# Performance work log

Hardware: AMD Instinct MI355X
Metric: run time of the kernel (lower is better)

Reference implementation:

```python
import jax, jax.numpy as jnp
import numpy as np

N_NODES = 50000
N_EDGES = 800000
DIMS = [128, 512, 256, 128]
EPS = 1e-5


def setup_inputs() -> dict:
    key = jax.random.key(0)
    ks = jax.random.split(key, 2 + 5 * 3)
    inp = {
        "x": jax.random.normal(ks[0], (N_NODES, DIMS[0]), dtype=jnp.float32),
        "edge_index": jax.random.randint(ks[1], (2, N_EDGES), 0, N_NODES, dtype=jnp.int64),
    }
    ki = 2
    for i in range(3):
        din, dout = DIMS[i], DIMS[i + 1]
        s = 1.0 / np.sqrt(din)
        inp[f"Wl{i}"] = jax.random.uniform(ks[ki + 0], (din, dout), jnp.float32, -s, s)
        inp[f"bl{i}"] = jax.random.uniform(ks[ki + 1], (dout,), jnp.float32, -s, s)
        inp[f"Wr{i}"] = jax.random.uniform(ks[ki + 2], (din, dout), jnp.float32, -s, s)
        inp[f"g{i}"] = jnp.ones((dout,), jnp.float32)
        inp[f"b{i}"] = jnp.zeros((dout,), jnp.float32)
        ki += 5
    return inp


def _sage_mean(x, src, dst, Wl, bl, Wr):
    n = x.shape[0]
    agg = jax.ops.segment_sum(x[src], dst, num_segments=n)  # [N, din]
    deg = jax.ops.segment_sum(jnp.ones((src.shape[0],), x.dtype), dst, num_segments=n)
    mean = agg / jnp.maximum(deg, 1.0)[:, None]
    return mean @ Wl + bl + x @ Wr


def _bn(h, gamma, beta):
    m = h.mean(axis=0)
    v = h.var(axis=0)
    return gamma * (h - m) * jax.lax.rsqrt(v + EPS) + beta


def reference(x, edge_index, Wl0, bl0, Wr0, g0, b0, Wl1, bl1, Wr1, g1, b1, Wl2, bl2, Wr2, g2, b2):
    src, dst = edge_index[0], edge_index[1]
    params = [(Wl0, bl0, Wr0, g0, b0), (Wl1, bl1, Wr1, g1, b1), (Wl2, bl2, Wr2, g2, b2)]
    h = x
    for Wl, bl, Wr, g, b in params:
        h = _sage_mean(h, src, dst, Wl, bl, Wr)
        h = _bn(h, g, b)
        h = jax.nn.relu(h)
        # dropout: identity in eval mode
    return h
```

## Files before the change

kernel.cpp:

```cpp
#include <hip/hip_runtime.h>
#include <cstdint>
#include <cstddef>


#define EPS_BN 1e-5f

typedef unsigned short ushort_t;
typedef __attribute__((ext_vector_type(8))) short short8;
typedef __attribute__((ext_vector_type(4))) float float4v;

__device__ __forceinline__ float bf2f(ushort_t u) {
    union { unsigned int i; float f; } v; v.i = ((unsigned int)u) << 16; return v.f;
}
__device__ __forceinline__ ushort_t f2bf(float f) {
    union { float f; unsigned int i; } v; v.f = f;
    unsigned int r = v.i + 0x7fffu + ((v.i >> 16) & 1u);
    return (ushort_t)(r >> 16);
}

__device__ __forceinline__ void async_copy16(void* lds, const void* g) {
    __builtin_amdgcn_global_load_lds(
        (const __attribute__((address_space(1))) unsigned int*)g,
        (__attribute__((address_space(3))) unsigned int*)lds, 16, 0, 0);
}

__global__ void detect_fmt_kernel(const int* __restrict__ edges, int* __restrict__ nz) {
    int t = threadIdx.x;
    int cnt = 0;
    #pragma unroll
    for (int j = 0; j < 4; ++j) {
        int idx = 2 * (t * 4 + j) + 1;
        if (edges[idx] != 0) cnt++;
    }
    if (cnt) atomicAdd(nz, cnt);
}

__device__ __forceinline__ void edge_sd(const int* __restrict__ p, int e, int ne,
                                        bool is64, int& s, int& d) {
    if (is64) { s = p[2 * e];  d = p[2 * ne + 2 * e]; }
    else      { s = p[e];      d = p[ne + e]; }
}

__global__ void count_deg_kernel(const int* __restrict__ edges, int ne,
                                 const int* __restrict__ nz, int* __restrict__ degi) {
    bool is64 = (*nz == 0);
    int e = blockIdx.x * 256 + threadIdx.x;
    if (e < ne) {
        int s, d; edge_sd(edges, e, ne, is64, s, d);
        atomicAdd(&degi[d], 1);
    }
}

__global__ void scan1_kernel(const int* __restrict__ degi, int n,
                             int* __restrict__ rowptr, int* __restrict__ bsums) {
    __shared__ int sh[1024];
    int t = threadIdx.x;
    int i = blockIdx.x * 1024 + t;
    int v = (i < n) ? degi[i] : 0;
    sh[t] = v;
    __syncthreads();
    for (int off = 1; off < 1024; off <<= 1) {
        int x = (t >= off) ? sh[t - off] : 0;
        __syncthreads();
        sh[t] += x;
        __syncthreads();
    }
    if (i < n) rowptr[i] = sh[t] - v;
    if (t == 1023) bsums[blockIdx.x] = sh[t];
}

__global__ void scan2_kernel(int* __restrict__ bsums, int nb,
                             int* __restrict__ rowptr, int n, int total) {
    if (threadIdx.x == 0 && blockIdx.x == 0) {
        int run = 0;
        for (int b = 0; b < nb; ++b) { int t = bsums[b]; bsums[b] = run; run += t; }
        rowptr[n] = total;
    }
}

__global__ void scan3_kernel(int* __restrict__ rowptr, int n,
                             const int* __restrict__ bsums, int* __restrict__ cursor) {
    int i = blockIdx.x * 1024 + threadIdx.x;
    if (i < n) {
        int v = rowptr[i] + bsums[blockIdx.x];
        rowptr[i] = v;
        cursor[i] = v;
    }
}

__global__ void scatter_kernel(const int* __restrict__ edges, int ne,
                               const int* __restrict__ nz,
                               int* __restrict__ cursor, int* __restrict__ csr_src) {
    bool is64 = (*nz == 0);
    int e = blockIdx.x * 256 + threadIdx.x;
    if (e < ne) {
        int s, d; edge_sd(edges, e, ne, is64, s, d);
        int pos = atomicAdd(&cursor[d], 1);
        csr_src[pos] = s;
    }
}

__global__ void f2b_kernel(const float* __restrict__ in, ushort_t* __restrict__ out, int n) {
    int i = blockIdx.x * 256 + threadIdx.x;
    if (i < n) out[i] = f2bf(in[i]);
}

__global__ void prep_wt_kernel(const float* __restrict__ Wl, const float* __restrict__ Wr,
                               ushort_t* __restrict__ WT, int K1, int Dout) {
    int idx = blockIdx.x * 256 + threadIdx.x;
    int K2 = 2 * K1;
    if (idx >= Dout * K2) return;
    int n = idx / K2, k = idx - n * K2;
    float v = (k < K1) ? Wl[(size_t)k * Dout + n] : Wr[(size_t)(k - K1) * Dout + n];
    WT[idx] = f2bf(v);
}

__global__ void prep_wtc_kernel(const float* __restrict__ Wl, const float* __restrict__ Wr,
                                ushort_t* __restrict__ WTc, int K, int D) {
    int idx = blockIdx.x * 256 + threadIdx.x;
    if (idx >= 2 * D * K) return;
    int nn = idx / K, k = idx - nn * K;
    float v = (nn < D) ? Wl[(size_t)k * D + nn] : Wr[(size_t)k * D + (nn - D)];
    WTc[idx] = f2bf(v);
}

template <int VEC> struct VecT;
template <> struct VecT<2> { using T = unsigned int; };
template <> struct VecT<4> { using T = uint2; };
template <> struct VecT<8> { using T = uint4; };

template <int VEC>
__device__ __forceinline__ void vunpack(typename VecT<VEC>::T v, unsigned int* w) {
    if constexpr (VEC == 2) { w[0] = v; }
    else if constexpr (VEC == 4) { w[0] = v.x; w[1] = v.y; }
    else { w[0] = v.x; w[1] = v.y; w[2] = v.z; w[3] = v.w; }
}

template <int VEC>
__device__ __forceinline__ void vaccum(typename VecT<VEC>::T v, float* acc) {
    unsigned int w[VEC / 2];
    vunpack<VEC>(v, w);
    #pragma unroll
    for (int i = 0; i < VEC / 2; ++i) {
        acc[2 * i + 0] += bf2f((ushort_t)(w[i] & 0xffffu));
        acc[2 * i + 1] += bf2f((ushort_t)(w[i] >> 16));
    }
}

template <int VEC>
__device__ __forceinline__ void gather_sum(
    const ushort_t* __restrict__ base, const int* __restrict__ csr_src,
    int e0, int e1, int rstride, float* acc) {
    using VT = typename VecT<VEC>::T;
    int e = e0;
    for (; e + 8 <= e1; e += 8) {
        VT v[8];
        #pragma unroll
        for (int u = 0; u < 8; ++u)
            v[u] = *(const VT*)(base + (size_t)csr_src[e + u] * rstride);
        #pragma unroll
        for (int u = 0; u < 8; ++u) vaccum<VEC>(v[u], acc);
    }
    if (e + 4 <= e1) {
        VT v[4];
        #pragma unroll
        for (int u = 0; u < 4; ++u)
            v[u] = *(const VT*)(base + (size_t)csr_src[e + u] * rstride);
        #pragma unroll
        for (int u = 0; u < 4; ++u) vaccum<VEC>(v[u], acc);
        e += 4;
    }
    if (e + 2 <= e1) {
        VT v0 = *(const VT*)(base + (size_t)csr_src[e] * rstride);
        VT v1 = *(const VT*)(base + (size_t)csr_src[e + 1] * rstride);
        vaccum<VEC>(v0, acc); vaccum<VEC>(v1, acc);
        e += 2;
    }
    if (e < e1)
        vaccum<VEC>(*(const VT*)(base + (size_t)csr_src[e] * rstride), acc);
}

template <int VEC>
__global__ __launch_bounds__(256) void aggregate_wave_kernel(
    const ushort_t* __restrict__ h, ushort_t* __restrict__ mean,
    const int* __restrict__ rowptr, const int* __restrict__ csr_src, int nnodes) {
    const int din = VEC * 64;
    int wid = blockIdx.x * 4 + (threadIdx.x >> 6);
    if (wid >= nnodes) return;
    int lane = threadIdx.x & 63;
    int e0 = rowptr[wid], e1 = rowptr[wid + 1];

    float acc[VEC];
    #pragma unroll
    for (int i = 0; i < VEC; ++i) acc[i] = 0.f;
    gather_sum<VEC>(h + (size_t)lane * VEC, csr_src, e0, e1, din, acc);

    int deg = e1 - e0;
    float scale = 1.0f / (float)(deg > 1 ? deg : 1);
    unsigned int o[VEC / 2];
    #pragma unroll
    for (int i = 0; i < VEC / 2; ++i)
        o[i] = (unsigned int)f2bf(acc[2 * i] * scale) |
               ((unsigned int)f2bf(acc[2 * i + 1] * scale) << 16);
    using VT = typename VecT<VEC>::T;
    VT ov;
    if constexpr (VEC == 2) { ov = o[0]; }
    else if constexpr (VEC == 4) { ov.x = o[0]; ov.y = o[1]; }
    else { ov.x = o[0]; ov.y = o[1]; ov.z = o[2]; ov.w = o[3]; }
    *(VT*)(mean + (size_t)wid * din + (size_t)lane * VEC) = ov;
}

template <int VEC>
__global__ __launch_bounds__(256) void aggregate_add_kernel(
    const ushort_t* __restrict__ PR, const float* __restrict__ bias,
    ushort_t* __restrict__ pre,
    const int* __restrict__ rowptr, const int* __restrict__ csr_src, int nnodes) {
    const int D = VEC * 64;
    const int stride = 2 * D;
    int wid = blockIdx.x * 4 + (threadIdx.x >> 6);
    if (wid >= nnodes) return;
    int lane = threadIdx.x & 63;
    int e0 = rowptr[wid], e1 = rowptr[wid + 1];

    float acc[VEC];
    #pragma unroll
    for (int i = 0; i < VEC; ++i) acc[i] = 0.f;
    gather_sum<VEC>(PR + (size_t)lane * VEC, csr_src, e0, e1, stride, acc);

    int deg = e1 - e0;
    float scale = 1.0f / (float)(deg > 1 ? deg : 1);

    using VT = typename VecT<VEC>::T;
    VT rv = *(const VT*)(PR + (size_t)wid * stride + D + (size_t)lane * VEC);
    unsigned int rw[VEC / 2];
    vunpack<VEC>(rv, rw);
    float o[VEC];
    #pragma unroll
    for (int i = 0; i < VEC / 2; ++i) {
        o[2 * i + 0] = bf2f((ushort_t)(rw[i] & 0xffffu));
        o[2 * i + 1] = bf2f((ushort_t)(rw[i] >> 16));
    }
    #pragma unroll
    for (int i = 0; i < VEC; ++i)
        o[i] += acc[i] * scale + bias[lane * VEC + i];

    unsigned int ow[VEC / 2];
    #pragma unroll
    for (int i = 0; i < VEC / 2; ++i)
        ow[i] = (unsigned int)f2bf(o[2 * i]) | ((unsigned int)f2bf(o[2 * i + 1]) << 16);
    VT ov;
    if constexpr (VEC == 2) { ov = ow[0]; }
    else if constexpr (VEC == 4) { ov.x = ow[0]; ov.y = ow[1]; }
    else { ov.x = ow[0]; ov.y = ow[1]; ov.z = ow[2]; ov.w = ow[3]; }
    *(VT*)(pre + (size_t)wid * D + (size_t)lane * VEC) = ov;
}

template <bool DUAL, bool BIAS>
__global__ __launch_bounds__(256) void gemm_glds_kernel(
    const ushort_t* __restrict__ A1, const ushort_t* __restrict__ A2,
    const ushort_t* __restrict__ BT, const float* __restrict__ bias,
    ushort_t* __restrict__ Cb, int N, int K1, int Ktot, int Wtot) {
    __shared__ ushort_t As[128 * 32];
    __shared__ ushort_t Bs[128 * 32];

    const int tid = threadIdx.x;
    const int wave = tid >> 6;
    const int lane = tid & 63;
    const int quad = lane >> 4;
    const int l15 = lane & 15;
    const int rowBase = blockIdx.y * 128;
    const int colBase = blockIdx.x * 128;
    const int wm = (wave >> 1) * 64;
    const int wn = (wave & 1) * 64;
    const int swz = (l15 >> 1) & 3;

    float4v acc[4][4];
    #pragma unroll
    for (int i = 0; i < 4; ++i)
        #pragma unroll
        for (int j = 0; j < 4; ++j)
            acc[i][j] = (float4v){0.f, 0.f, 0.f, 0.f};

    const int nkt = Ktot / 32;
    const int khalf = K1 / 32;

    for (int kt = 0; kt < nkt; ++kt) {
        const ushort_t* Asrc = A1;
        int kg = kt * 32;
        if (DUAL && kt >= khalf) { Asrc = A2; kg = (kt - khalf) * 32; }
        const int kb = kt * 32;

        #pragma unroll
        for (int u = 0; u < 2; ++u) {
            int c = u * 256 + tid;
            int r = c >> 2;
            int off = (((c & 3) ^ ((c >> 3) & 3)) * 8);
            int grow = rowBase + r;
            if (grow >= N) grow = N - 1;
            async_copy16(&As[c * 8], Asrc + (size_t)grow * K1 + kg + off);
            async_copy16(&Bs[c * 8], BT + (size_t)(colBase + r) * Ktot + kb + off);
        }
        __syncthreads();

        short8 af[4], bf4[4];
        #pragma unroll
        for (int i = 0; i < 4; ++i)
            af[i] = *(const short8*)&As[(wm + i * 16 + l15) * 32 + (quad ^ swz) * 8];
        #pragma unroll
        for (int j = 0; j < 4; ++j)
            bf4[j] = *(const short8*)&Bs[(wn + j * 16 + l15) * 32 + (quad ^ swz) * 8];

        #pragma unroll
        for (int i = 0; i < 4; ++i)
            #pragma unroll
            for (int j = 0; j < 4; ++j)
                acc[i][j] = __builtin_amdgcn_mfma_f32_16x16x32_bf16(bf4[j], af[i], acc[i][j], 0, 0, 0);
        __syncthreads();
    }

    ushort_t* lws = (wave < 2) ? &As[wave * 2048] : &Bs[(wave - 2) * 2048];
    #pragma unroll
    for (int p = 0; p < 2; ++p) {
        #pragma unroll
        for (int jj = 0; jj < 2; ++jj) {
            int j = 2 * p + jj;
            float4 bv = make_float4(0.f, 0.f, 0.f, 0.f);
            if (BIAS) bv = *(const float4*)(bias + colBase + wn + j * 16 + quad * 4);
            #pragma unroll
            for (int i = 0; i < 4; ++i) {
                uint2 pk;
                pk.x = (unsigned int)f2bf(acc[i][j][0] + bv.x) |
                       ((unsigned int)f2bf(acc[i][j][1] + bv.y) << 16);
                pk.y = (unsigned int)f2bf(acc[i][j][2] + bv.z) |
                       ((unsigned int)f2bf(acc[i][j][3] + bv.w) << 16);
                *(uint2*)&lws[(i * 16 + l15) * 32 + jj * 16 + quad * 4] = pk;
            }
        }
        __syncthreads();
        #pragma unroll
        for (int it = 0; it < 4; ++it) {
            int c = it * 64 + lane;
            int row = c >> 2, coff = (c & 3) * 8;
            int grow = rowBase + wm + row;
            if (grow < N) {
                uint4 v = *(const uint4*)&lws[row * 32 + coff];
                *(uint4*)(Cb + (size_t)grow * Wtot + colBase + wn + p * 32 + coff) = v;
            }
        }
        __syncthreads();
    }
}

__global__ void colstats_b_kernel(const ushort_t* __restrict__ h, int N, int D,
                                  float* __restrict__ sum, float* __restrict__ sumsq) {
    int c2 = blockIdx.x * 128 + (threadIdx.x & 63) * 2;
    int rl = threadIdx.x >> 6;
    float s0 = 0.f, s20 = 0.f, s1 = 0.f, s21 = 0.f;
    int stride = gridDim.y * 4;
    for (int r = blockIdx.y * 4 + rl; r < N; r += stride) {
        unsigned int w = *(const unsigned int*)(h + (size_t)r * D + c2);
        float v0 = bf2f((ushort_t)(w & 0xffffu));
        float v1 = bf2f((ushort_t)(w >> 16));
        s0 += v0; s20 += v0 * v0;
        s1 += v1; s21 += v1 * v1;
    }
    atomicAdd(&sum[c2 + 0], s0);
    atomicAdd(&sumsq[c2 + 0], s20);
    atomicAdd(&sum[c2 + 1], s1);
    atomicAdd(&sumsq[c2 + 1], s21);
}

__global__ void bn_relu_b2b_kernel(const ushort_t* __restrict__ h, ushort_t* __restrict__ hb,
                                   int N, int D,
                                   const float* __restrict__ sum, const float* __restrict__ sumsq,
                                   const float* __restrict__ g, const float* __restrict__ b) {
    size_t idx = (size_t)blockIdx.x * blockDim.x + threadIdx.x;
    size_t tot = (size_t)N * D / 2;
    if (idx >= tot) return;
    int cp = (int)(idx & (size_t)(D / 2 - 1));
    int c0 = cp * 2, c1 = c0 + 1;
    float m0 = sum[c0] / (float)N, m1 = sum[c1] / (float)N;
    float i0 = rsqrtf(sumsq[c0] / (float)N - m0 * m0 + EPS_BN);
    float i1 = rsqrtf(sumsq[c1] / (float)N - m1 * m1 + EPS_BN);
    unsigned int w = ((const unsigned int*)h)[idx];
    float v0 = g[c0] * (bf2f((ushort_t)(w & 0xffffu)) - m0) * i0 + b[c0];
    float v1 = g[c1] * (bf2f((ushort_t)(w >> 16)) - m1) * i1 + b[c1];
    v0 = v0 > 0.f ? v0 : 0.f;
    v1 = v1 > 0.f ? v1 : 0.f;
    ((unsigned int*)hb)[idx] = (unsigned int)f2bf(v0) | ((unsigned int)f2bf(v1) << 16);
}

__global__ void bn_relu_b2f_kernel(const ushort_t* __restrict__ h, float* __restrict__ hf,
                                   int N, int D,
                                   const float* __restrict__ sum, const float* __restrict__ sumsq,
                                   const float* __restrict__ g, const float* __restrict__ b) {
    size_t idx = (size_t)blockIdx.x * blockDim.x + threadIdx.x;
    size_t tot = (size_t)N * D / 2;
    if (idx >= tot) return;
    int cp = (int)(idx & (size_t)(D / 2 - 1));
    int c0 = cp * 2, c1 = c0 + 1;
    float m0 = sum[c0] / (float)N, m1 = sum[c1] / (float)N;
    float i0 = rsqrtf(sumsq[c0] / (float)N - m0 * m0 + EPS_BN);
    float i1 = rsqrtf(sumsq[c1] / (float)N - m1 * m1 + EPS_BN);
    unsigned int w = ((const unsigned int*)h)[idx];
    float v0 = g[c0] * (bf2f((ushort_t)(w & 0xffffu)) - m0) * i0 + b[c0];
    float v1 = g[c1] * (bf2f((ushort_t)(w >> 16)) - m1) * i1 + b[c1];
    float2 o;
    o.x = v0 > 0.f ? v0 : 0.f;
    o.y = v1 > 0.f ? v1 : 0.f;
    *(float2*)(hf + idx * 2) = o;
}

extern "C" void kernel_launch(void* const* d_in, const int* in_sizes, int n_in,
                              void* d_out, int out_size, void* d_ws, size_t ws_size,
                              hipStream_t stream) {
    const float* x     = (const float*)d_in[0];
    const int*   edges = (const int*)d_in[1];
    const float* Wl0 = (const float*)d_in[2];
    const float* bl0 = (const float*)d_in[3];
    const float* Wr0 = (const float*)d_in[4];
    const float* g0  = (const float*)d_in[5];
    const float* b0  = (const float*)d_in[6];
    const float* Wl1 = (const float*)d_in[7];
    const float* bl1 = (const float*)d_in[8];
    const float* Wr1 = (const float*)d_in[9];
    const float* g1  = (const float*)d_in[10];
    const float* b1  = (const float*)d_in[11];
    const float* Wl2 = (const float*)d_in[12];
    const float* bl2 = (const float*)d_in[13];
    const float* Wr2 = (const float*)d_in[14];
    const float* g2  = (const float*)d_in[15];
    const float* b2  = (const float*)d_in[16];

    const int D0 = 128, D1 = 512, D2 = 256, D3 = 128;
    const int n  = in_sizes[0] / D0;
    const int ne = in_sizes[1] / 2;

    char* base = (char*)d_ws;
    size_t off = 0;
    auto alloc = [&](size_t bytes) -> char* {
        char* p = base + off;
        off = (off + bytes + 255) & ~(size_t)255;
        return p;
    };
    int*      nzflag  = (int*)alloc(4);
    int*      degi    = (int*)alloc((size_t)n * 4);
    float*    stats   = (float*)alloc(6 * 512 * 4);
    size_t    zero_span = off;
    int*      rowptr  = (int*)alloc((size_t)(n + 1) * 4);
    int*      cursor  = (int*)alloc((size_t)n * 4);
    int*      csr_src = (int*)alloc((size_t)ne * 4);
    int*      bsums   = (int*)alloc(64 * 4);
    ushort_t* xb      = (ushort_t*)alloc((size_t)n * D0 * 2);
    ushort_t* mb      = (ushort_t*)alloc((size_t)n * 512 * 2);
    ushort_t* h1b     = (ushort_t*)alloc((size_t)n * D1 * 2);
    ushort_t* h2b     = (ushort_t*)alloc((size_t)n * D2 * 2);
    ushort_t* hpre    = (ushort_t*)alloc((size_t)n * 512 * 2);
    ushort_t* WT0     = (ushort_t*)alloc((size_t)D1 * 2 * D0 * 2);
    ushort_t* WT1c    = (ushort_t*)alloc((size_t)(2 * D2) * D1 * 2);
    ushort_t* WT2c    = (ushort_t*)alloc((size_t)(2 * D3) * D2 * 2);
    float*    out     = (float*)d_out;
    (void)ws_size; (void)n_in; (void)out_size;

    hipMemsetAsync(base, 0, zero_span, stream);

    detect_fmt_kernel<<<1, 256, 0, stream>>>(edges, nzflag);
    count_deg_kernel<<<(ne + 255) / 256, 256, 0, stream>>>(edges, ne, nzflag, degi);
    int nscan = (n + 1023) / 1024;
    scan1_kernel<<<nscan, 1024, 0, stream>>>(degi, n, rowptr, bsums);
    scan2_kernel<<<1, 64, 0, stream>>>(bsums, nscan, rowptr, n, ne);
    scan3_kernel<<<nscan, 1024, 0, stream>>>(rowptr, n, bsums, cursor);
    scatter_kernel<<<(ne + 255) / 256, 256, 0, stream>>>(edges, ne, nzflag, cursor, csr_src);

    f2b_kernel<<<((size_t)n * D0 + 255) / 256, 256, 0, stream>>>(x, xb, n * D0);
    prep_wt_kernel<<<(D1 * 2 * D0 + 255) / 256, 256, 0, stream>>>(Wl0, Wr0, WT0, D0, D1);
    prep_wtc_kernel<<<(2 * D2 * D1 + 255) / 256, 256, 0, stream>>>(Wl1, Wr1, WT1c, D1, D2);
    prep_wtc_kernel<<<(2 * D3 * D2 + 255) / 256, 256, 0, stream>>>(Wl2, Wr2, WT2c, D2, D3);

    const int aggGrid = (n + 3) / 4;
    const int rowBlocks = (n + 127) / 128;
    float* st0 = stats + 0 * 1024;
    float* st1 = stats + 1 * 1024;
    float* st2 = stats + 2 * 1024;

    aggregate_wave_kernel<2><<<aggGrid, 256, 0, stream>>>(xb, mb, rowptr, csr_src, n);
    gemm_glds_kernel<true, true><<<dim3(D1 / 128, rowBlocks), 256, 0, stream>>>(
        mb, xb, WT0, bl0, hpre, n, D0, 2 * D0, D1);
    colstats_b_kernel<<<dim3(D1 / 128, 128), 256, 0, stream>>>(hpre, n, D1, st0, st0 + 512);
    bn_relu_b2b_kernel<<<((size_t)n * D1 / 2 + 255) / 256, 256, 0, stream>>>(
        hpre, h1b, n, D1, st0, st0 + 512, g0, b0);

    gemm_glds_kernel<false, false><<<dim3(2 * D2 / 128, rowBlocks), 256, 0, stream>>>(
        h1b, nullptr, WT1c, nullptr, mb, n, D1, D1, 2 * D2);
    aggregate_add_kernel<4><<<aggGrid, 256, 0, stream>>>(
        mb, bl1, hpre, rowptr, csr_src, n);
    colstats_b_kernel<<<dim3(D2 / 128, 128), 256, 0, stream>>>(hpre, n, D2, st1, st1 + 512);
    bn_relu_b2b_kernel<<<((size_t)n * D2 / 2 + 255) / 256, 256, 0, stream>>>(
        hpre, h2b, n, D2, st1, st1 + 512, g1, b1);

    gemm_glds_kernel<false, false><<<dim3(2 * D3 / 128, rowBlocks), 256, 0, stream>>>(
        h2b, nullptr, WT2c, nullptr, mb, n, D2, D2, 2 * D3);
    aggregate_add_kernel<2><<<aggGrid, 256, 0, stream>>>(
        mb, bl2, hpre, rowptr, csr_src, n);
    colstats_b_kernel<<<dim3(D3 / 128, 128), 256, 0, stream>>>(hpre, n, D3, st2, st2 + 512);
    bn_relu_b2f_kernel<<<((size_t)n * D3 / 2 + 255) / 256, 256, 0, stream>>>(
        hpre, out, n, D3, st2, st2 + 512, g2, b2);
}
```

Baseline: 666.0 us.

## Build CSR via two-level bucket sort and widen GEMM K-tile to 64

Replaces the global-atomic degree count, three-kernel scan and per-edge atomic scatter with a bucketed counting sort. Edges are grouped by dst>>8 using LDS histograms, packed with the low dst bits, and each bucket is then sorted locally to produce rowptr and csr_src. This cuts global atomic contention and kernel launches. Separately, the GEMM K-tile grows from 32 to 64 with a wider XOR swizzle, halving the barrier count per K, at the cost of doubled LDS use and lower occupancy. The packing assumes source indices fit in 24 bits and at most 256 buckets, so n is limited to about 65536.

```diff
diff --git a/kernel.cpp b/kernel.cpp
--- a/kernel.cpp
+++ b/kernel.cpp
@@ -40,63 +40,116 @@
     if (is64) { s = p[2 * e];  d = p[2 * ne + 2 * e]; }
     else      { s = p[e];      d = p[ne + e]; }
 }
-
-__global__ void count_deg_kernel(const int* __restrict__ edges, int ne,
-                                 const int* __restrict__ nz, int* __restrict__ degi) {
+__device__ __forceinline__ int edge_d(const int* __restrict__ p, int e, int ne, bool is64) {
+    return is64 ? p[2 * ne + 2 * e] : p[ne + e];
+}
+
+#define EPB 2048
+
+__global__ __launch_bounds__(256) void bhist_kernel(
+    const int* __restrict__ edges, int ne, const int* __restrict__ nz,
+    int* __restrict__ gcnt) {
+    __shared__ int h[256];
+    int t = threadIdx.x;
+    h[t] = 0;
+    __syncthreads();
     bool is64 = (*nz == 0);
-    int e = blockIdx.x * 256 + threadIdx.x;
-    if (e < ne) {
-        int s, d; edge_sd(edges, e, ne, is64, s, d);
-        atomicAdd(&degi[d], 1);
-    }
-}
-
-__global__ void scan1_kernel(const int* __restrict__ degi, int n,
-                             int* __restrict__ rowptr, int* __restrict__ bsums) {
-    __shared__ int sh[1024];
+    int base_e = blockIdx.x * EPB;
+    #pragma unroll
+    for (int u = 0; u < EPB / 256; ++u) {
+        int i = base_e + u * 256 + t;
+        if (i < ne) atomicAdd(&h[edge_d(edges, i, ne, is64) >> 8], 1);
+    }
+    __syncthreads();
+    if (h[t]) atomicAdd(&gcnt[t], h[t]);
+}
+
+__global__ __launch_bounds__(256) void bscan_kernel(
+    const int* __restrict__ gcnt, int nb, int ne,
+    int* __restrict__ bbase, int* __restrict__ bcur) {
+    __shared__ int sh[256];
     int t = threadIdx.x;
-    int i = blockIdx.x * 1024 + t;
-    int v = (i < n) ? degi[i] : 0;
+    int v = (t < nb) ? gcnt[t] : 0;
     sh[t] = v;
     __syncthreads();
-    for (int off = 1; off < 1024; off <<= 1) {
-        int x = (t >= off) ? sh[t - off] : 0;
+    for (int o = 1; o < 256; o <<= 1) {
+        int x = (t >= o) ? sh[t - o] : 0;
         __syncthreads();
         sh[t] += x;
         __syncthreads();
     }
-    if (i < n) rowptr[i] = sh[t] - v;
-    if (t == 1023) bsums[blockIdx.x] = sh[t];
-}
-
-__global__ void scan2_kernel(int* __restrict__ bsums, int nb,
-                             int* __restrict__ rowptr, int n, int total) {
-    if (threadIdx.x == 0 && blockIdx.x == 0) {
-        int run = 0;
-        for (int b = 0; b < nb; ++b) { int t = bsums[b]; bsums[b] = run; run += t; }
-        rowptr[n] = total;
-    }
-}
-
-__global__ void scan3_kernel(int* __restrict__ rowptr, int n,
-                             const int* __restrict__ bsums, int* __restrict__ cursor) {
-    int i = blockIdx.x * 1024 + threadIdx.x;
-    if (i < n) {
-        int v = rowptr[i] + bsums[blockIdx.x];
-        rowptr[i] = v;
-        cursor[i] = v;
-    }
-}
-
-__global__ void scatter_kernel(const int* __restrict__ edges, int ne,
-                               const int* __restrict__ nz,
-                               int* __restrict__ cursor, int* __restrict__ csr_src) {
+    int excl = sh[t] - v;
+    if (t < nb) { bbase[t] = excl; bcur[t] = excl; }
+    if (t == nb) bbase[t] = ne;
+    if (nb == 256 && t == 0) {  }
+    if (t == 0 && nb == 256) bbase[256] = ne;
+}
+
+__global__ __launch_bounds__(256) void bscatter_kernel(
+    const int* __restrict__ edges, int ne, const int* __restrict__ nz,
+    int* __restrict__ bcur, int* __restrict__ packed) {
+    __shared__ int h[256];
+    __shared__ int chunkb[256];
+    __shared__ int lcur[256];
+    int t = threadIdx.x;
+    h[t] = 0;
+    lcur[t] = 0;
+    __syncthreads();
     bool is64 = (*nz == 0);
-    int e = blockIdx.x * 256 + threadIdx.x;
-    if (e < ne) {
-        int s, d; edge_sd(edges, e, ne, is64, s, d);
-        int pos = atomicAdd(&cursor[d], 1);
-        csr_src[pos] = s;
+    int base_e = blockIdx.x * EPB;
+    int ent[EPB / 256], eb[EPB / 256];
+    #pragma unroll
+    for (int u = 0; u < EPB / 256; ++u) {
+        int i = base_e + u * 256 + t;
+        if (i < ne) {
+            int s, d;
+            edge_sd(edges, i, ne, is64, s, d);
+            ent[u] = s | ((d & 255) << 24);
+            eb[u] = d >> 8;
+            atomicAdd(&h[eb[u]], 1);
+        } else eb[u] = -1;
+    }
+    __syncthreads();
+    if (h[t]) chunkb[t] = atomicAdd(&bcur[t], h[t]);
+    __syncthreads();
+    #pragma unroll
+    for (int u = 0; u < EPB / 256; ++u) {
+        if (eb[u] >= 0) {
+            int lp = atomicAdd(&lcur[eb[u]], 1);
+            packed[chunkb[eb[u]] + lp] = ent[u];
+        }
+    }
+}
+
+__global__ __launch_bounds__(256) void bbuild_kernel(
+    const int* __restrict__ packed, const int* __restrict__ bbase,
+    int* __restrict__ rowptr, int* __restrict__ csr_src, int n) {
+    __shared__ int h[256];
+    __shared__ int cur[256];
+    int t = threadIdx.x;
+    int bb = blockIdx.x;
+    int base = bbase[bb], cnt = bbase[bb + 1] - base;
+    h[t] = 0;
+    __syncthreads();
+    for (int i = t; i < cnt; i += 256)
+        atomicAdd(&h[(unsigned)packed[base + i] >> 24], 1);
+    __syncthreads();
+    int v = h[t];
+    for (int o = 1; o < 256; o <<= 1) {
+        int x = (t >= o) ? h[t - o] : 0;
+        __syncthreads();
+        h[t] += x;
+        __syncthreads();
+    }
+    int excl = h[t] - v;
+    int node = bb * 256 + t;
+    if (node <= n) rowptr[node] = base + excl;
+    cur[t] = excl;
+    __syncthreads();
+    for (int i = t; i < cnt; i += 256) {
+        int e = packed[base + i];
+        int lp = atomicAdd(&cur[(unsigned)e >> 24], 1);
+        csr_src[base + lp] = e & 0xffffff;
     }
 }
 
@@ -260,19 +313,19 @@
     const ushort_t* __restrict__ A1, const ushort_t* __restrict__ A2,
     const ushort_t* __restrict__ BT, const float* __restrict__ bias,
     ushort_t* __restrict__ Cb, int N, int K1, int Ktot, int Wtot) {
-    __shared__ ushort_t As[128 * 32];
-    __shared__ ushort_t Bs[128 * 32];
+    __shared__ ushort_t As[128 * 64];
+    __shared__ ushort_t Bs[128 * 64];
 
     const int tid = threadIdx.x;
     const int wave = tid >> 6;
     const int lane = tid & 63;
     const int quad = lane >> 4;
     const int l15 = lane & 15;
+    const int sw7 = l15 & 7;
     const int rowBase = blockIdx.y * 128;
     const int colBase = blockIdx.x * 128;
     const int wm = (wave >> 1) * 64;
     const int wn = (wave & 1) * 64;
-    const int swz = (l15 >> 1) & 3;
 
     float4v acc[4][4];
     #pragma unroll
@@ -281,20 +334,20 @@
         for (int j = 0; j < 4; ++j)
             acc[i][j] = (float4v){0.f, 0.f, 0.f, 0.f};
 
-    const int nkt = Ktot / 32;
-    const int khalf = K1 / 32;
+    const int nkt = Ktot / 64;
+    const int khalf = K1 / 64;
 
     for (int kt = 0; kt < nkt; ++kt) {
         const ushort_t* Asrc = A1;
-        int kg = kt * 32;
-        if (DUAL && kt >= khalf) { Asrc = A2; kg = (kt - khalf) * 32; }
-        const int kb = kt * 32;
-
-        #pragma unroll
-        for (int u = 0; u < 2; ++u) {
+        int kg = kt * 64;
+        if (DUAL && kt >= khalf) { Asrc = A2; kg = (kt - khalf) * 64; }
+        const int kb = kt * 64;
+
+        #pragma unroll
+        for (int u = 0; u < 4; ++u) {
             int c = u * 256 + tid;
-            int r = c >> 2;
-            int off = (((c & 3) ^ ((c >> 3) & 3)) * 8);
+            int r = c >> 3, cc = c & 7;
+            int off = (cc ^ (r & 7)) * 8;
             int grow = rowBase + r;
             if (grow >= N) grow = N - 1;
             async_copy16(&As[c * 8], Asrc + (size_t)grow * K1 + kg + off);
@@ -302,23 +355,26 @@
         }
         __syncthreads();
 
-        short8 af[4], bf4[4];
-        #pragma unroll
-        for (int i = 0; i < 4; ++i)
-            af[i] = *(const short8*)&As[(wm + i * 16 + l15) * 32 + (quad ^ swz) * 8];
-        #pragma unroll
-        for (int j = 0; j < 4; ++j)
-            bf4[j] = *(const short8*)&Bs[(wn + j * 16 + l15) * 32 + (quad ^ swz) * 8];
-
-        #pragma unroll
-        for (int i = 0; i < 4; ++i)
+        #pragma unroll
+        for (int kh = 0; kh < 2; ++kh) {
+            int cidx = kh * 4 + quad;
+            short8 af[4], bf4[4];
+            #pragma unroll
+            for (int i = 0; i < 4; ++i)
+                af[i] = *(const short8*)&As[(wm + i * 16 + l15) * 64 + (cidx ^ sw7) * 8];
             #pragma unroll
             for (int j = 0; j < 4; ++j)
-                acc[i][j] = __builtin_amdgcn_mfma_f32_16x16x32_bf16(bf4[j], af[i], acc[i][j], 0, 0, 0);
-        __syncthreads();
-    }
-
-    ushort_t* lws = (wave < 2) ? &As[wave * 2048] : &Bs[(wave - 2) * 2048];
+                bf4[j] = *(const short8*)&Bs[(wn + j * 16 + l15) * 64 + (cidx ^ sw7) * 8];
+            #pragma unroll
+            for (int i = 0; i < 4; ++i)
+                #pragma unroll
+                for (int j = 0; j < 4; ++j)
+                    acc[i][j] = __builtin_amdgcn_mfma_f32_16x16x32_bf16(bf4[j], af[i], acc[i][j], 0, 0, 0);
+        }
+        __syncthreads();
+    }
+
+    ushort_t* lws = &As[wave * 2048];
     #pragma unroll
     for (int p = 0; p < 2; ++p) {
         #pragma unroll
@@ -435,6 +491,7 @@
     const int D0 = 128, D1 = 512, D2 = 256, D3 = 128;
     const int n  = in_sizes[0] / D0;
     const int ne = in_sizes[1] / 2;
+    const int NB = (n + 255) >> 8;
 
     char* base = (char*)d_ws;
     size_t off = 0;
@@ -444,13 +501,14 @@
         return p;
     };
     int*      nzflag  = (int*)alloc(4);
-    int*      degi    = (int*)alloc((size_t)n * 4);
+    int*      gcnt    = (int*)alloc(256 * 4);
     float*    stats   = (float*)alloc(6 * 512 * 4);
     size_t    zero_span = off;
+    int*      bbase   = (int*)alloc(257 * 4);
+    int*      bcur    = (int*)alloc(256 * 4);
+    int*      packed  = (int*)alloc((size_t)ne * 4);
     int*      rowptr  = (int*)alloc((size_t)(n + 1) * 4);
-    int*      cursor  = (int*)alloc((size_t)n * 4);
     int*      csr_src = (int*)alloc((size_t)ne * 4);
-    int*      bsums   = (int*)alloc(64 * 4);
     ushort_t* xb      = (ushort_t*)alloc((size_t)n * D0 * 2);
     ushort_t* mb      = (ushort_t*)alloc((size_t)n * 512 * 2);
     ushort_t* h1b     = (ushort_t*)alloc((size_t)n * D1 * 2);
@@ -465,12 +523,11 @@
     hipMemsetAsync(base, 0, zero_span, stream);
 
     detect_fmt_kernel<<<1, 256, 0, stream>>>(edges, nzflag);
-    count_deg_kernel<<<(ne + 255) / 256, 256, 0, stream>>>(edges, ne, nzflag, degi);
-    int nscan = (n + 1023) / 1024;
-    scan1_kernel<<<nscan, 1024, 0, stream>>>(degi, n, rowptr, bsums);
-    scan2_kernel<<<1, 64, 0, stream>>>(bsums, nscan, rowptr, n, ne);
-    scan3_kernel<<<nscan, 1024, 0, stream>>>(rowptr, n, bsums, cursor);
-    scatter_kernel<<<(ne + 255) / 256, 256, 0, stream>>>(edges, ne, nzflag, cursor, csr_src);
+    int ablk = (ne + EPB - 1) / EPB;
+    bhist_kernel<<<ablk, 256, 0, stream>>>(edges, ne, nzflag, gcnt);
+    bscan_kernel<<<1, 256, 0, stream>>>(gcnt, NB, ne, bbase, bcur);
+    bscatter_kernel<<<ablk, 256, 0, stream>>>(edges, ne, nzflag, bcur, packed);
+    bbuild_kernel<<<NB, 256, 0, stream>>>(packed, bbase, rowptr, csr_src, n);
 
     f2b_kernel<<<((size_t)n * D0 + 255) / 256, 256, 0, stream>>>(x, xb, n * D0);
     prep_wt_kernel<<<(D1 * 2 * D0 + 255) / 256, 256, 0, stream>>>(Wl0, Wr0, WT0, D0, D1);
```

After: 596.7 us. 10.4% less time.
